# Kernel tuning notes

Hardware: AMD Instinct MI355X
Metric: run time of the kernel (lower is better)

The kernel has to match this reference:

```python
import jax, jax.numpy as jnp
import numpy as np

HIDDEN = 32
FUTURE = 6
B, T, F = 256, 2048, 64


def setup_inputs() -> dict:
    key = jax.random.key(0)
    k1, k2, k3, k4 = jax.random.split(key, 4)
    s_x = 1.0 / np.sqrt(F)
    s_h = 1.0 / np.sqrt(HIDDEN)
    return {
        "X_batch": jax.random.normal(k1, (B, T, F), dtype=jnp.float32),
        # stacked input->gates kernel, gate order (i, f, g, o), no input bias (flax dense_i use_bias=False)
        "Wx": jax.random.normal(k2, (F, 4 * HIDDEN), dtype=jnp.float32) * s_x,
        # stacked hidden->gates kernel + bias (flax dense_h use_bias=True)
        "Wh": jax.random.normal(k3, (HIDDEN, 4 * HIDDEN), dtype=jnp.float32) * s_h,
        "b": jnp.zeros((4 * HIDDEN,), dtype=jnp.float32),
        # output head Dense(future)
        "Wd": jax.random.normal(k4, (HIDDEN, FUTURE), dtype=jnp.float32) * s_h,
        "bd": jnp.zeros((FUTURE,), dtype=jnp.float32),
    }


def reference(X_batch, Wx, Wh, b, Wd, bd):
    Bsz = X_batch.shape[0]
    H = HIDDEN

    # Precompute input projection for all timesteps in one big GEMM: [B,T,4H]
    x_proj = jnp.einsum("btf,fg->btg", X_batch, Wx) + b
    xs = jnp.swapaxes(x_proj, 0, 1)  # [T, B, 4H]

    def step(carry, xg):
        c, h = carry
        z = xg + h @ Wh  # [B, 4H]
        i = jax.nn.sigmoid(z[:, 0 * H:1 * H])
        f = jax.nn.sigmoid(z[:, 1 * H:2 * H])
        g = jnp.tanh(z[:, 2 * H:3 * H])
        o = jax.nn.sigmoid(z[:, 3 * H:4 * H])
        c = f * c + i * g
        h = o * jnp.tanh(c)
        return (c, h), None

    init = (jnp.zeros((Bsz, H), X_batch.dtype), jnp.zeros((Bsz, H), X_batch.dtype))
    (c_T, h_T), _ = jax.lax.scan(step, init, xs)

    # original applies elu + Dense(6) to the whole sequence then takes x[:, -1, :];
    # mathematically identical to applying the head to the final hidden state only.
    out = jax.nn.elu(h_T) @ Wd + bd  # [B, FUTURE]
    return out
```

## Files before the change

kernel.cpp:

```cpp
#include <hip/hip_runtime.h>

#define FOUR_H 128
#define FUT 6
#define BSZ 256
#define TT 2048
#define FF 64
#define CH 16
#define NCH (TT / CH)

typedef float f32x2 __attribute__((ext_vector_type(2)));
typedef float f32x4 __attribute__((ext_vector_type(4)));
typedef unsigned int u32;
typedef u32 u32x4 __attribute__((ext_vector_type(4)));
typedef short bf16x8 __attribute__((ext_vector_type(8)));

__device__ __forceinline__ float fast_rcp(float x)  { return __builtin_amdgcn_rcpf(x); }
__device__ __forceinline__ float fast_exp2(float x) { return __builtin_amdgcn_exp2f(x); }
__device__ __forceinline__ float sigmoid_f(float x) {
    float t = fast_exp2(x * -1.44269504088896340736f);
    return fast_rcp(1.0f + t);
}
__device__ __forceinline__ u32 f2u(float x) { return __builtin_bit_cast(u32, x); }
__device__ __forceinline__ float u2f(u32 x) { return __builtin_bit_cast(float, x); }

__device__ __forceinline__ void gload_lds16(const void* g, void* l) {
    __builtin_amdgcn_global_load_lds(
        (const __attribute__((address_space(1))) void*)g,
        (__attribute__((address_space(3))) void*)l, 16, 0, 0);
}

__device__ __forceinline__ f32x4 mfma16(bf16x8 a, bf16x8 b, f32x4 c) {
    return __builtin_amdgcn_mfma_f32_16x16x32_bf16(a, b, c, 0, 0, 0);
}

__global__ __launch_bounds__(128) void lstm_fused(
    const float* __restrict__ X, const float* __restrict__ Wx,
    const float* __restrict__ bias, const float* __restrict__ Wh,
    const float* __restrict__ Wd, const float* __restrict__ bd,
    float* __restrict__ out)
{
    __shared__ float xstage[2 * CH * FF];
    __shared__ float zbuf[2 * CH * FOUR_H];
    __shared__ u32x4 wfrag[8 * 2 * 2 * 64];
    __shared__ float sh[32];

    int wv = threadIdx.x >> 6;
    int b  = blockIdx.x;
    int l  = threadIdx.x & 63;
    int kl = l & 31;
    int lr = l >> 4;
    int lc = l & 15;
    bool lowHalf = (l < 32);

    const u32 PSEL = 0x07060302u;
    const char* Xb = (const char*)(X + (size_t)b * TT * FF);

    f32x2 wh0p[16], wh1p[16];
    float c = 0.0f, h = 0.0f;
    const float4* shq = (const float4*)sh;
    const float L2E = 1.44269504088896340736f;
    float s1 = lowHalf ? (-2.0f * L2E) : (-L2E);
    float m1 = lowHalf ? 2.0f : 1.0f;
    float a1 = lowHalf ? -1.0f : 0.0f;

    float bj[8];
    int soff[4];

    if (wv == 0) {
#pragma unroll
        for (int m = 0; m < 16; ++m) {
            wh0p[m][0] = Wh[(2 * m) * FOUR_H + l];
            wh0p[m][1] = Wh[(2 * m + 1) * FOUR_H + l];
            wh1p[m][0] = Wh[(2 * m) * FOUR_H + 64 + l];
            wh1p[m][1] = Wh[(2 * m + 1) * FOUR_H + 64 + l];
        }
    } else {
#pragma unroll
        for (int n = 0; n < 8; ++n) bj[n] = bias[n * 16 + lc];
#pragma unroll
        for (int i = 0; i < 4; ++i) {
            int t = i * 4 + lr;
            soff[i] = t * 256 + ((lc ^ t) << 4);
        }
#pragma unroll 2
        for (int n = 0; n < 8; ++n)
            for (int ks = 0; ks < 2; ++ks) {
                u32 hi[4], lo[4];
#pragma unroll
                for (int e = 0; e < 4; ++e) {
                    int k0 = ks * 32 + lr * 8 + 2 * e;
                    float w0 = Wx[k0 * FOUR_H + n * 16 + lc];
                    float w1 = Wx[(k0 + 1) * FOUR_H + n * 16 + lc];
                    u32 x0 = f2u(w0), x1 = f2u(w1);
                    hi[e] = __builtin_amdgcn_perm(x1, x0, PSEL);
                    float l0 = w0 - u2f(x0 & 0xFFFF0000u);
                    float l1 = w1 - u2f(x1 & 0xFFFF0000u);
                    lo[e] = __builtin_amdgcn_perm(f2u(l1), f2u(l0), PSEL);
                }
                wfrag[((n * 2 + ks) * 2 + 0) * 64 + l] = (u32x4){hi[0], hi[1], hi[2], hi[3]};
                wfrag[((n * 2 + ks) * 2 + 1) * 64 + l] = (u32x4){lo[0], lo[1], lo[2], lo[3]};
            }
    }

#define GLOAD(mm)                                                            \
    {                                                                        \
        const char* src = Xb + (size_t)(mm) * 4096;                          \
        char* dst = (char*)xstage + ((mm) & 1) * 4096;                       \
        _Pragma("unroll")                                                    \
        for (int i = 0; i < 4; ++i)                                          \
            gload_lds16(src + soff[i], dst + i * 1024);                      \
    }

#define ZPREP(mm)                                                            \
    {                                                                        \
        f32x4 zacc[8];                                                       \
        _Pragma("unroll")                                                    \
        for (int n = 0; n < 8; ++n)                                          \
            zacc[n] = (f32x4){bj[n], bj[n], bj[n], bj[n]};                   \
        const char* xs = (const char*)xstage + ((mm) & 1) * 4096;            \
        _Pragma("unroll")                                                    \
        for (int ks = 0; ks < 2; ++ks) {                                     \
            int q0 = ks * 8 + lr * 2;                                        \
            int aoff = lc * 256 + ((q0 ^ lc) << 4);                          \
            u32x4 xa = *(const u32x4*)(xs + aoff);                           \
            u32x4 xv = *(const u32x4*)(xs + (aoff ^ 16));                    \
            u32 h0 = __builtin_amdgcn_perm(xa.y, xa.x, PSEL);                \
            u32 h1 = __builtin_amdgcn_perm(xa.w, xa.z, PSEL);                \
            u32 h2 = __builtin_amdgcn_perm(xv.y, xv.x, PSEL);                \
            u32 h3 = __builtin_amdgcn_perm(xv.w, xv.z, PSEL);                \
            float d0 = u2f(xa.x) - u2f(xa.x & 0xFFFF0000u);                  \
            float d1 = u2f(xa.y) - u2f(xa.y & 0xFFFF0000u);                  \
            float d2 = u2f(xa.z) - u2f(xa.z & 0xFFFF0000u);                  \
            float d3 = u2f(xa.w) - u2f(xa.w & 0xFFFF0000u);                  \
            float d4 = u2f(xv.x) - u2f(xv.x & 0xFFFF0000u);                  \
            float d5 = u2f(xv.y) - u2f(xv.y & 0xFFFF0000u);                  \
            float d6 = u2f(xv.z) - u2f(xv.z & 0xFFFF0000u);                  \
            float d7 = u2f(xv.w) - u2f(xv.w & 0xFFFF0000u);                  \
            u32 g0 = __builtin_amdgcn_perm(f2u(d1), f2u(d0), PSEL);          \
            u32 g1 = __builtin_amdgcn_perm(f2u(d3), f2u(d2), PSEL);          \
            u32 g2 = __builtin_amdgcn_perm(f2u(d5), f2u(d4), PSEL);          \
            u32 g3 = __builtin_amdgcn_perm(f2u(d7), f2u(d6), PSEL);          \
            bf16x8 ahi = __builtin_bit_cast(bf16x8, (u32x4){h0, h1, h2, h3});\
            bf16x8 alo = __builtin_bit_cast(bf16x8, (u32x4){g0, g1, g2, g3});\
            _Pragma("unroll")                                                \
            for (int n = 0; n < 8; ++n) {                                    \
                bf16x8 bh = __builtin_bit_cast(bf16x8,                       \
                    wfrag[((n * 2 + ks) * 2 + 0) * 64 + l]);                 \
                bf16x8 bl = __builtin_bit_cast(bf16x8,                       \
                    wfrag[((n * 2 + ks) * 2 + 1) * 64 + l]);                 \
                zacc[n] = mfma16(ahi, bh, zacc[n]);                          \
                zacc[n] = mfma16(ahi, bl, zacc[n]);                          \
                zacc[n] = mfma16(alo, bh, zacc[n]);                          \
            }                                                                \
        }                                                                    \
        f32x4* zo = (f32x4*)zbuf + ((mm) & 1) * 512 + lr * 128 + lc;         \
        _Pragma("unroll")                                                    \
        for (int n = 0; n < 8; ++n) zo[n * 16] = zacc[n];                    \
    }

#define STEP_BODY(Z0, Z1)                                                    \
    {                                                                        \
        sh[kl] = h;                                                          \
        float4 hq[8];                                                        \
        _Pragma("unroll")                                                    \
        for (int q = 0; q < 8; ++q) hq[q] = shq[q];                          \
        f32x2 a0 = {(Z0), 0.0f}, b0 = {0.0f, 0.0f};                          \
        f32x2 a1v = {(Z1), 0.0f}, b1 = {0.0f, 0.0f};                         \
        _Pragma("unroll")                                                    \
        for (int q = 0; q < 8; ++q) {                                        \
            f32x2 hlo = {hq[q].x, hq[q].y};                                  \
            f32x2 hhi = {hq[q].z, hq[q].w};                                  \
            a0  = __builtin_elementwise_fma(hlo, wh0p[2 * q],     a0);       \
            b0  = __builtin_elementwise_fma(hhi, wh0p[2 * q + 1], b0);       \
            a1v = __builtin_elementwise_fma(hlo, wh1p[2 * q],     a1v);      \
            b1  = __builtin_elementwise_fma(hhi, wh1p[2 * q + 1], b1);       \
        }                                                                    \
        f32x2 s0p = a0 + b0;                                                 \
        f32x2 s1p = a1v + b1;                                                \
        float A0 = s0p[0] + s0p[1];                                          \
        float A1 = s1p[0] + s1p[1];                                          \
        float act0 = sigmoid_f(A0);                                          \
        float u1 = fast_rcp(1.0f + fast_exp2(A1 * s1));                      \
        float act1 = fmaf(u1, m1, a1);                                       \
        float gi = act0, gf = act0;                                          \
        asm("v_permlane32_swap_b32 %0, %1" : "+v"(gi), "+v"(gf));            \
        float gg = act1, go = act1;                                          \
        asm("v_permlane32_swap_b32 %0, %1" : "+v"(gg), "+v"(go));            \
        c = fmaf(gf, c, gi * gg);                                            \
        float uc = fast_rcp(1.0f + fast_exp2(c * -2.88539008177792681472f)); \
        float tc2 = fmaf(uc, 2.0f, -1.0f);                                   \
        h = go * tc2;                                                        \
    }

    if (wv == 1) {
        GLOAD(0)
        GLOAD(1)
        asm volatile("s_waitcnt vmcnt(4)" ::: "memory");
        ZPREP(0)
    }
    __syncthreads();

    for (int m = 0; m < NCH; ++m) {
        if (wv == 1) {
            if (m + 1 < NCH) {
                if (m + 2 < NCH) {
                    GLOAD(m + 2)
                    asm volatile("s_waitcnt vmcnt(4)" ::: "memory");
                } else {
                    asm volatile("s_waitcnt vmcnt(0)" ::: "memory");
                }
                ZPREP(m + 1)
            }
        } else {
            const float4* zb = (const float4*)zbuf + (m & 1) * 512;
            float4 z0q[4], z1q[4];
#pragma unroll
            for (int u4 = 0; u4 < 4; ++u4) {
                z0q[u4] = zb[u4 * 128 + l];
                z1q[u4] = zb[u4 * 128 + 64 + l];
            }
#pragma unroll
            for (int u4 = 0; u4 < 4; ++u4) {
                STEP_BODY(z0q[u4].x, z1q[u4].x)
                STEP_BODY(z0q[u4].y, z1q[u4].y)
                STEP_BODY(z0q[u4].z, z1q[u4].z)
                STEP_BODY(z0q[u4].w, z1q[u4].w)
            }
        }
        __syncthreads();
    }

#undef STEP_BODY
#undef ZPREP
#undef GLOAD

    if (wv == 0) {
        float e = (h > 0.0f) ? h : (fast_exp2(h * L2E) - 1.0f);
#pragma unroll
        for (int q = 0; q < FUT; ++q) {
            float v = lowHalf ? e * Wd[kl * FUT + q] : 0.0f;
#pragma unroll
            for (int off = 1; off < 64; off <<= 1)
                v += __shfl_xor(v, off);
            if (l == 0) out[b * FUT + q] = v + bd[q];
        }
    }
}

extern "C" void kernel_launch(void* const* d_in, const int* in_sizes, int n_in,
                              void* d_out, int out_size, void* d_ws, size_t ws_size,
                              hipStream_t stream)
{
    const float* X    = (const float*)d_in[0];
    const float* Wx   = (const float*)d_in[1];
    const float* Wh   = (const float*)d_in[2];
    const float* bias = (const float*)d_in[3];
    const float* Wd   = (const float*)d_in[4];
    const float* bd   = (const float*)d_in[5];
    float* out = (float*)d_out;

    lstm_fused<<<dim3(BSZ), dim3(128), 0, stream>>>(X, Wx, bias, Wh, Wd, bd, out);
}
```

Before: 348.9 us.

## Pack two sequences per block and keep Wx fragments in registers

The kernel now launches half as many blocks of 512 threads, each handling two batch rows. Each row gets its own recurrence wave and projection wave, and two waves per row sit idle. The Wx bf16 hi/lo MFMA fragments move from shared memory into per-thread registers of the projection wave, which removes LDS reads from the input-projection loop. The trade-offs are fewer active CUs, two latency-bound recurrence waves possibly sharing a SIMD, a block-wide barrier now coupling two sequences, and higher register pressure.

```diff
diff --git a/kernel.cpp b/kernel.cpp
--- a/kernel.cpp
+++ b/kernel.cpp
@@ -33,20 +33,21 @@
     return __builtin_amdgcn_mfma_f32_16x16x32_bf16(a, b, c, 0, 0, 0);
 }
 
-__global__ __launch_bounds__(128) void lstm_fused(
+__global__ __launch_bounds__(512) void lstm_fused(
     const float* __restrict__ X, const float* __restrict__ Wx,
     const float* __restrict__ bias, const float* __restrict__ Wh,
     const float* __restrict__ Wd, const float* __restrict__ bd,
     float* __restrict__ out)
 {
-    __shared__ float xstage[2 * CH * FF];
-    __shared__ float zbuf[2 * CH * FOUR_H];
-    __shared__ u32x4 wfrag[8 * 2 * 2 * 64];
-    __shared__ float sh[32];
-
-    int wv = threadIdx.x >> 6;
-    int b  = blockIdx.x;
-    int l  = threadIdx.x & 63;
+    __shared__ float xstage[2][2 * CH * FF];
+    __shared__ float zbuf[2][2 * CH * FOUR_H];
+    __shared__ float sh[2][32];
+
+    int wv   = threadIdx.x >> 6;
+    int role = wv & 3;
+    int ci   = wv >> 2;
+    int b    = blockIdx.x * 2 + ci;
+    int l    = threadIdx.x & 63;
     int kl = l & 31;
     int lr = l >> 4;
     int lc = l & 15;
@@ -55,9 +56,13 @@
     const u32 PSEL = 0x07060302u;
     const char* Xb = (const char*)(X + (size_t)b * TT * FF);
 
+    float* xstageC = xstage[ci];
+    float* zbufC   = zbuf[ci];
+    float* shC     = sh[ci];
+    const float4* shq = (const float4*)shC;
+
     f32x2 wh0p[16], wh1p[16];
     float c = 0.0f, h = 0.0f;
-    const float4* shq = (const float4*)sh;
     const float L2E = 1.44269504088896340736f;
     float s1 = lowHalf ? (-2.0f * L2E) : (-L2E);
     float m1 = lowHalf ? 2.0f : 1.0f;
@@ -65,8 +70,9 @@
 
     float bj[8];
     int soff[4];
-
-    if (wv == 0) {
+    u32x4 wregH[16], wregL[16];
+
+    if (role == 0) {
 #pragma unroll
         for (int m = 0; m < 16; ++m) {
             wh0p[m][0] = Wh[(2 * m) * FOUR_H + l];
@@ -74,7 +80,7 @@
             wh1p[m][0] = Wh[(2 * m) * FOUR_H + 64 + l];
             wh1p[m][1] = Wh[(2 * m + 1) * FOUR_H + 64 + l];
         }
-    } else {
+    } else if (role == 1) {
 #pragma unroll
         for (int n = 0; n < 8; ++n) bj[n] = bias[n * 16 + lc];
 #pragma unroll
@@ -97,15 +103,15 @@
                     float l1 = w1 - u2f(x1 & 0xFFFF0000u);
                     lo[e] = __builtin_amdgcn_perm(f2u(l1), f2u(l0), PSEL);
                 }
-                wfrag[((n * 2 + ks) * 2 + 0) * 64 + l] = (u32x4){hi[0], hi[1], hi[2], hi[3]};
-                wfrag[((n * 2 + ks) * 2 + 1) * 64 + l] = (u32x4){lo[0], lo[1], lo[2], lo[3]};
+                wregH[n * 2 + ks] = (u32x4){hi[0], hi[1], hi[2], hi[3]};
+                wregL[n * 2 + ks] = (u32x4){lo[0], lo[1], lo[2], lo[3]};
             }
     }
 
 #define GLOAD(mm)                                                            \
     {                                                                        \
         const char* src = Xb + (size_t)(mm) * 4096;                          \
-        char* dst = (char*)xstage + ((mm) & 1) * 4096;                       \
+        char* dst = (char*)xstageC + ((mm) & 1) * 4096;                      \
         _Pragma("unroll")                                                    \
         for (int i = 0; i < 4; ++i)                                          \
             gload_lds16(src + soff[i], dst + i * 1024);                      \
@@ -117,7 +123,7 @@
         _Pragma("unroll")                                                    \
         for (int n = 0; n < 8; ++n)                                          \
             zacc[n] = (f32x4){bj[n], bj[n], bj[n], bj[n]};                   \
-        const char* xs = (const char*)xstage + ((mm) & 1) * 4096;            \
+        const char* xs = (const char*)xstageC + ((mm) & 1) * 4096;           \
         _Pragma("unroll")                                                    \
         for (int ks = 0; ks < 2; ++ks) {                                     \
             int q0 = ks * 8 + lr * 2;                                        \
@@ -144,23 +150,21 @@
             bf16x8 alo = __builtin_bit_cast(bf16x8, (u32x4){g0, g1, g2, g3});\
             _Pragma("unroll")                                                \
             for (int n = 0; n < 8; ++n) {                                    \
-                bf16x8 bh = __builtin_bit_cast(bf16x8,                       \
-                    wfrag[((n * 2 + ks) * 2 + 0) * 64 + l]);                 \
-                bf16x8 bl = __builtin_bit_cast(bf16x8,                       \
-                    wfrag[((n * 2 + ks) * 2 + 1) * 64 + l]);                 \
+                bf16x8 bh = __builtin_bit_cast(bf16x8, wregH[n * 2 + ks]);   \
+                bf16x8 bl = __builtin_bit_cast(bf16x8, wregL[n * 2 + ks]);   \
                 zacc[n] = mfma16(ahi, bh, zacc[n]);                          \
                 zacc[n] = mfma16(ahi, bl, zacc[n]);                          \
                 zacc[n] = mfma16(alo, bh, zacc[n]);                          \
             }                                                                \
         }                                                                    \
-        f32x4* zo = (f32x4*)zbuf + ((mm) & 1) * 512 + lr * 128 + lc;         \
+        f32x4* zo = (f32x4*)zbufC + ((mm) & 1) * 512 + lr * 128 + lc;        \
         _Pragma("unroll")                                                    \
         for (int n = 0; n < 8; ++n) zo[n * 16] = zacc[n];                    \
     }
 
 #define STEP_BODY(Z0, Z1)                                                    \
     {                                                                        \
-        sh[kl] = h;                                                          \
+        shC[kl] = h;                                                         \
         float4 hq[8];                                                        \
         _Pragma("unroll")                                                    \
         for (int q = 0; q < 8; ++q) hq[q] = shq[q];                          \
@@ -192,7 +196,7 @@
         h = go * tc2;                                                        \
     }
 
-    if (wv == 1) {
+    if (role == 1) {
         GLOAD(0)
         GLOAD(1)
         asm volatile("s_waitcnt vmcnt(4)" ::: "memory");
@@ -201,7 +205,7 @@
     __syncthreads();
 
     for (int m = 0; m < NCH; ++m) {
-        if (wv == 1) {
+        if (role == 1) {
             if (m + 1 < NCH) {
                 if (m + 2 < NCH) {
                     GLOAD(m + 2)
@@ -211,8 +215,8 @@
                 }
                 ZPREP(m + 1)
             }
-        } else {
-            const float4* zb = (const float4*)zbuf + (m & 1) * 512;
+        } else if (role == 0) {
+            const float4* zb = (const float4*)zbufC + (m & 1) * 512;
             float4 z0q[4], z1q[4];
 #pragma unroll
             for (int u4 = 0; u4 < 4; ++u4) {
@@ -234,7 +238,7 @@
 #undef ZPREP
 #undef GLOAD
 
-    if (wv == 0) {
+    if (role == 0) {
         float e = (h > 0.0f) ? h : (fast_exp2(h * L2E) - 1.0f);
 #pragma unroll
         for (int q = 0; q < FUT; ++q) {
@@ -259,5 +263,5 @@
     const float* bd   = (const float*)d_in[5];
     float* out = (float*)d_out;
 
-    lstm_fused<<<dim3(BSZ), dim3(128), 0, stream>>>(X, Wx, bias, Wh, Wd, bd, out);
-}
+    lstm_fused<<<dim3(BSZ / 2), dim3(512), 0, stream>>>(X, Wx, bias, Wh, Wd, bd, out);
+}
```

After: 575.5 us. 65.0% more time.
